# Performance work log

Hardware: AMD Instinct MI355X
Metric: run time of the kernel (lower is better)

The kernel has to match this reference:

```python
import jax, jax.numpy as jnp
import numpy as np

# --- module constants (from init_kwargs) ---
CIN, COUT = 16, 8
HIN = WIN = 8
K, S, P, OP = 3, 2, 1, 1
GRID_SIZE, SPLINE_ORDER = 5, 3
HOUT = (HIN - 1) * S - 2 * P + K + OP  # 16
WOUT = HOUT
OH_IN = (HIN + 2 * P - K) // S + 1   # 4
OW_IN = OH_IN
OH_OUT = (HOUT + 2 * P - K) // S + 1  # 8
OW_OUT = OH_OUT
IN_F = CIN * K * K * OH_IN * OW_IN    # 2304
OUT_F = COUT * K * K * OH_OUT * OW_OUT  # 4608
B = 64


def make_grid():
    h = (1.0 - (-1.0)) / GRID_SIZE
    g = jnp.arange(-SPLINE_ORDER, GRID_SIZE + SPLINE_ORDER + 1, dtype=jnp.float32) * h - 1.0
    return jnp.broadcast_to(g, (IN_F, g.shape[0]))  # [in_features, G+2k+1]


def unfold(x):
    # x: [B, C, H, W] -> [B, C*K*K, OH*OW], torch F.unfold ordering (C, kh, kw) x (oh, ow)
    b, c, h, w = x.shape
    xp = jnp.pad(x, ((0, 0), (0, 0), (P, P), (P, P)))
    oh = (h + 2 * P - K) // S + 1
    ow = (w + 2 * P - K) // S + 1
    patches = jnp.stack(
        [xp[:, :, i:i + (oh - 1) * S + 1:S, j:j + (ow - 1) * S + 1:S]
         for i in range(K) for j in range(K)], axis=2)  # [B, C, K*K, oh, ow]
    return patches.reshape(b, c * K * K, oh * ow)


def fold(u, out_h, out_w):
    # u: [B, C*K*K, oh*ow] -> scatter-add -> [B, C, out_h, out_w] (torch F.fold)
    b = u.shape[0]
    c = u.shape[1] // (K * K)
    oh = (out_h + 2 * P - K) // S + 1
    ow = (out_w + 2 * P - K) // S + 1
    u = u.reshape(b, c, K, K, oh, ow)
    out = jnp.zeros((b, c, out_h + 2 * P, out_w + 2 * P), dtype=u.dtype)
    for i in range(K):
        for j in range(K):
            out = out.at[:, :, i:i + (oh - 1) * S + 1:S, j:j + (ow - 1) * S + 1:S].add(u[:, :, i, j])
    return out[:, :, P:out_h + P, P:out_w + P]


def b_splines(x2, grid):
    # x2: [N, in_f], grid: [in_f, G+2k+1] -> [N, in_f, G+k]
    xg = x2[:, :, None]
    bases = ((xg >= grid[:, :-1]) & (xg < grid[:, 1:])).astype(x2.dtype)
    for k in range(1, SPLINE_ORDER + 1):
        bases = ((xg - grid[:, :-(k + 1)]) / (grid[:, k:-1] - grid[:, :-(k + 1)]) * bases[:, :, :-1]
                 + (grid[:, k + 1:] - xg) / (grid[:, k + 1:] - grid[:, 1:-k]) * bases[:, :, 1:])
    return bases


def setup_inputs() -> dict:
    key = jax.random.key(0)
    k1, k2, k3, k4 = jax.random.split(key, 4)
    return {
        "x": jax.random.normal(k1, (B, CIN, HIN, WIN), dtype=jnp.float32),
        "base_weight": jax.random.normal(k2, (OUT_F, IN_F), dtype=jnp.float32) * 0.02,
        "spline_weight": jax.random.normal(k3, (OUT_F, IN_F, GRID_SIZE + SPLINE_ORDER), dtype=jnp.float32) * 0.02,
        "spline_scaler": jax.random.normal(k4, (OUT_F, IN_F), dtype=jnp.float32) * 0.02,
        "grid": make_grid(),
    }


def reference(x, base_weight, spline_weight, spline_scaler, grid):
    u = unfold(x).reshape(-1, IN_F)  # [B, in_features]
    # KANLinear: base path (SiLU + linear) + spline path
    base_out = jax.nn.silu(u) @ base_weight.T  # [B, out_f]
    scaled_w = (spline_weight * spline_scaler[:, :, None]).reshape(OUT_F, -1)
    spline_out = b_splines(u, grid).reshape(u.shape[0], -1) @ scaled_w.T
    y = (base_out + spline_out).reshape(-1, COUT * K * K, OH_OUT * OW_OUT)
    return fold(y, HOUT, WOUT)  # [B, COUT, HOUT, WOUT]
```

## Files before the change

### kernel.cpp

```cpp
#include <hip/hip_runtime.h>

#define CIN   16
#define COUTC 8
#define HIN   8
#define WINW  8
#define SST   2
#define PPD   1
#define HOUTC 16
#define WOUTC 16
#define IN_F  2304
#define OUT_F 4608
#define BATCH 64

#define OS    8
#define FC    (IN_F / OS)
#define SF    16
#define NSUB  (FC / SF)
#define NWAVE 3

typedef __bf16 bf16x8 __attribute__((ext_vector_type(8)));
typedef float  f32x4  __attribute__((ext_vector_type(4)));

__device__ __forceinline__ float gridv(int t) {
    return (float)(t - 3) * 0.4f - 1.0f;
}

__device__ __forceinline__ void gload_lds16(const float* g, float* l) {
    __builtin_amdgcn_global_load_lds(
        (const __attribute__((address_space(1))) unsigned int*)g,
        (__attribute__((address_space(3))) unsigned int*)l, 16, 0, 0);
}

__global__ __launch_bounds__(256) void prep_kernel(const float* __restrict__ x,
                                                   __bf16* __restrict__ Abb,
                                                   __bf16* __restrict__ Bsb) {
    int tid = blockIdx.x * 256 + threadIdx.x;
    if (tid >= IN_F * BATCH) return;
    int f = tid >> 6, b = tid & 63;
    int ckk = f >> 4, s = f & 15;
    int c = ckk / 9, r = ckk % 9;
    int ki = r / 3, kj = r % 3;
    int oh = s >> 2, ow = s & 3;
    int h = ki + oh * SST - PPD;
    int w = kj + ow * SST - PPD;
    float u = 0.0f;
    if (h >= 0 && h < HIN && w >= 0 && w < WINW)
        u = x[((b * CIN + c) * HIN + h) * WINW + w];

    {
        size_t idx = ((size_t)((f >> 5) * 4 + (b >> 4))) * 512
                   + (((f >> 3) & 3) * 16 + (b & 15)) * 8 + (f & 7);
        Abb[idx] = (__bf16)(u / (1.0f + __expf(-u)));
    }

    float bs[11];
#pragma unroll
    for (int t = 0; t < 11; ++t)
        bs[t] = (u >= gridv(t) && u < gridv(t + 1)) ? 1.0f : 0.0f;
#pragma unroll
    for (int k = 1; k <= 3; ++k) {
#pragma unroll
        for (int i = 0; i < 11; ++i) {
            if (i < 11 - k) {
                float g_i  = gridv(i);
                float g_ik = gridv(i + k);
                float g_i1 = gridv(i + 1);
                float g_k1 = gridv(i + k + 1);
                bs[i] = (u - g_i) / (g_ik - g_i) * bs[i]
                      + (g_k1 - u) / (g_k1 - g_i1) * bs[i + 1];
            }
        }
    }
    bf16x8 v;
#pragma unroll
    for (int t = 0; t < 8; ++t) v[t] = (__bf16)bs[t];
    size_t frag = ((size_t)((f >> 2) * 4 + (b >> 4))) * 64
                + (f & 3) * 16 + (b & 15);
    ((bf16x8*)Bsb)[frag] = v;
}

__global__ __launch_bounds__(192, 2) void gemm_kernel(
    const float* __restrict__ Wb,
    const float* __restrict__ Ws,
    const float* __restrict__ Sc,
    const __bf16* __restrict__ Abb,
    const __bf16* __restrict__ Bsb,
    float* __restrict__ partial)
{
    __shared__ __align__(16) char smem[2 * 16384 + 2 * 4096];
    char* splb = smem;
    char* scb  = smem + 32768;

    const int tid  = threadIdx.x;
    const int lane = tid & 63;
    const int wv   = tid >> 6;
    const int lr   = lane & 15;
    const int lg   = lane >> 4;
    const int ot = blockIdx.x / OS;
    const int os = blockIdx.x % OS;
    const int o0 = ot * 48;
    const int f0 = os * FC;
    const int o  = o0 + wv * 16 + lr;

    f32x4 acc0 = {0.f,0.f,0.f,0.f}, acc1 = {0.f,0.f,0.f,0.f};
    f32x4 acc2 = {0.f,0.f,0.f,0.f}, acc3 = {0.f,0.f,0.f,0.f};

    auto stage = [&](int t, int pb) {
        const char* src = (const char*)Bsb + ((size_t)(f0 + t * SF) >> 2) * 4096;
        char* dst = splb + pb * 16384;
        for (int i = wv; i < 16; i += NWAVE)
            gload_lds16((const float*)(src + i * 1024) + lane * 4,
                        (float*)(dst + i * 1024));
        const int r = wv * 16 + (lane >> 2);
        gload_lds16(Sc + (size_t)(o0 + r) * IN_F + f0 + t * SF + (lane & 3) * 4,
                    (float*)(scb + pb * 4096 + wv * 1024));
    };

    const float* wp = Ws + ((size_t)o * IN_F + f0 + lg) * 8;

    stage(0, 0);
    __syncthreads();

    for (int t = 0; t < NSUB; ++t) {
        const int pb = t & 1;
        if (t + 1 < NSUB) stage(t + 1, pb ^ 1);

        const char*  ab  = splb + pb * 16384;
        const float* scl = (const float*)(scb + pb * 4096);
#pragma unroll
        for (int s = 0; s < SF / 4; ++s) {
            const int fs = t * SF + s * 4;
            float4 w0 = *(const float4*)(wp + (size_t)fs * 8);
            float4 w1 = *(const float4*)(wp + (size_t)fs * 8 + 4);
            float  sc = scl[(wv * 16 + lr) * 16 + s * 4 + lg];
            bf16x8 b0 = *(const bf16x8*)(ab + s * 4096 +    0 + lane * 16);
            bf16x8 b1 = *(const bf16x8*)(ab + s * 4096 + 1024 + lane * 16);
            bf16x8 b2 = *(const bf16x8*)(ab + s * 4096 + 2048 + lane * 16);
            bf16x8 b3 = *(const bf16x8*)(ab + s * 4096 + 3072 + lane * 16);
            bf16x8 af;
            af[0] = (__bf16)(w0.x * sc); af[1] = (__bf16)(w0.y * sc);
            af[2] = (__bf16)(w0.z * sc); af[3] = (__bf16)(w0.w * sc);
            af[4] = (__bf16)(w1.x * sc); af[5] = (__bf16)(w1.y * sc);
            af[6] = (__bf16)(w1.z * sc); af[7] = (__bf16)(w1.w * sc);
            acc0 = __builtin_amdgcn_mfma_f32_16x16x32_bf16(af, b0, acc0, 0, 0, 0);
            acc1 = __builtin_amdgcn_mfma_f32_16x16x32_bf16(af, b1, acc1, 0, 0, 0);
            acc2 = __builtin_amdgcn_mfma_f32_16x16x32_bf16(af, b2, acc2, 0, 0, 0);
            acc3 = __builtin_amdgcn_mfma_f32_16x16x32_bf16(af, b3, acc3, 0, 0, 0);
        }
        __syncthreads();
    }

    const float*  wbp = Wb + (size_t)o * IN_F + f0 + lg * 8;
    const bf16x8* ap  = (const bf16x8*)Abb + ((size_t)f0 >> 5) * 256 + lane;
#pragma unroll
    for (int s = 0; s < FC / 32; ++s) {
        float4 w0 = *(const float4*)(wbp + s * 32);
        float4 w1 = *(const float4*)(wbp + s * 32 + 4);
        bf16x8 b0 = ap[s * 256 +   0];
        bf16x8 b1 = ap[s * 256 +  64];
        bf16x8 b2 = ap[s * 256 + 128];
        bf16x8 b3 = ap[s * 256 + 192];
        bf16x8 af;
        af[0] = (__bf16)w0.x; af[1] = (__bf16)w0.y;
        af[2] = (__bf16)w0.z; af[3] = (__bf16)w0.w;
        af[4] = (__bf16)w1.x; af[5] = (__bf16)w1.y;
        af[6] = (__bf16)w1.z; af[7] = (__bf16)w1.w;
        acc0 = __builtin_amdgcn_mfma_f32_16x16x32_bf16(af, b0, acc0, 0, 0, 0);
        acc1 = __builtin_amdgcn_mfma_f32_16x16x32_bf16(af, b1, acc1, 0, 0, 0);
        acc2 = __builtin_amdgcn_mfma_f32_16x16x32_bf16(af, b2, acc2, 0, 0, 0);
        acc3 = __builtin_amdgcn_mfma_f32_16x16x32_bf16(af, b3, acc3, 0, 0, 0);
    }

#pragma unroll
    for (int r = 0; r < 4; ++r) {
        const size_t row = (size_t)os * OUT_F + o0 + wv * 16 + lg * 4 + r;
        partial[row * 64 +  0 + lr] = acc0[r];
        partial[row * 64 + 16 + lr] = acc1[r];
        partial[row * 64 + 32 + lr] = acc2[r];
        partial[row * 64 + 48 + lr] = acc3[r];
    }
}

__global__ __launch_bounds__(256) void fold_kernel(const float* __restrict__ partial,
                                                   float* __restrict__ out) {
    int gid = blockIdx.x * 256 + threadIdx.x;
    int b = gid & 63, p = gid >> 6;
    int w = p & 15, h = (p >> 4) & 15, c = p >> 8;
    float sum = 0.0f;
#pragma unroll
    for (int ki = 0; ki < 3; ++ki) {
        int th = h + 1 - ki;
        if (th < 0 || (th & 1) || (th >> 1) >= 8) continue;
        int oh = th >> 1;
#pragma unroll
        for (int kj = 0; kj < 3; ++kj) {
            int tw = w + 1 - kj;
            if (tw < 0 || (tw & 1) || (tw >> 1) >= 8) continue;
            int ow = tw >> 1;
            int o = ((c * 3 + ki) * 3 + kj) * 64 + oh * 8 + ow;
            const float* pp = partial + (size_t)o * 64 + b;
#pragma unroll
            for (int os = 0; os < OS; ++os)
                sum += pp[(size_t)os * (OUT_F * 64)];
        }
    }
    out[((b * COUTC + c) * HOUTC + h) * WOUTC + w] = sum;
}

extern "C" void kernel_launch(void* const* d_in, const int* in_sizes, int n_in,
                              void* d_out, int out_size, void* d_ws, size_t ws_size,
                              hipStream_t stream) {
    const float* x  = (const float*)d_in[0];
    const float* Wb = (const float*)d_in[1];
    const float* Ws = (const float*)d_in[2];
    const float* Sc = (const float*)d_in[3];

    float* out = (float*)d_out;

    __bf16* Abb     = (__bf16*)d_ws;
    __bf16* Bsb     = Abb + (size_t)IN_F * BATCH;
    float*  partial = (float*)(Bsb + (size_t)IN_F * BATCH * 8);

    prep_kernel<<<(IN_F * BATCH + 255) / 256, 256, 0, stream>>>(x, Abb, Bsb);

    gemm_kernel<<<(OUT_F / 48) * OS, 192, 0, stream>>>(Wb, Ws, Sc, Abb, Bsb, partial);

    fold_kernel<<<(BATCH * COUTC * HOUTC * WOUTC) / 256, 256, 0, stream>>>(partial, out);
}
```

Measured before the change: 104.2 us.

## Double split-K factor, halve sub-tile, and raise GEMM occupancy

Doubles the K-split from 8 to 16 slices and halves the per-step feature chunk, so the grid has twice as many GEMM blocks and each block uses less LDS. Launch bounds now allow 5 blocks per SIMD instead of 2. The scaler tile is loaded once every two sub-steps and double-buffered separately, and the base-path 32-feature blocks are spread unevenly (5 or 4 per slice) because 72 blocks do not divide by 16. The aim is more memory parallelism on the bandwidth-bound weight stream. The cost is twice the partial-sum traffic written by the GEMM and read back by the fold kernel.

```diff
diff --git a/kernel.cpp b/kernel.cpp
--- a/kernel.cpp
+++ b/kernel.cpp
@@ -12,9 +12,9 @@
 #define OUT_F 4608
 #define BATCH 64
 
-#define OS    8
+#define OS    16
 #define FC    (IN_F / OS)
-#define SF    16
+#define SF    8
 #define NSUB  (FC / SF)
 #define NWAVE 3
 
@@ -79,7 +79,7 @@
     ((bf16x8*)Bsb)[frag] = v;
 }
 
-__global__ __launch_bounds__(192, 2) void gemm_kernel(
+__global__ __launch_bounds__(192, 5) void gemm_kernel(
     const float* __restrict__ Wb,
     const float* __restrict__ Ws,
     const float* __restrict__ Sc,
@@ -87,9 +87,9 @@
     const __bf16* __restrict__ Bsb,
     float* __restrict__ partial)
 {
-    __shared__ __align__(16) char smem[2 * 16384 + 2 * 4096];
-    char* splb = smem;
-    char* scb  = smem + 32768;
+    __shared__ __align__(16) char smem[2 * 8192 + 2 * 3072];
+    char*  splb = smem;
+    float* scb  = (float*)(smem + 16384);
 
     const int tid  = threadIdx.x;
     const int lane = tid & 63;
@@ -105,34 +105,39 @@
     f32x4 acc0 = {0.f,0.f,0.f,0.f}, acc1 = {0.f,0.f,0.f,0.f};
     f32x4 acc2 = {0.f,0.f,0.f,0.f}, acc3 = {0.f,0.f,0.f,0.f};
 
-    auto stage = [&](int t, int pb) {
-        const char* src = (const char*)Bsb + ((size_t)(f0 + t * SF) >> 2) * 4096;
-        char* dst = splb + pb * 16384;
-        for (int i = wv; i < 16; i += NWAVE)
+    auto stage_act = [&](int t, int pb) {
+        const char* src = (const char*)Bsb + (size_t)(f0 + t * SF) * 1024;
+        char* dst = splb + pb * 8192;
+        for (int i = wv; i < 8; i += NWAVE)
             gload_lds16((const float*)(src + i * 1024) + lane * 4,
                         (float*)(dst + i * 1024));
+    };
+    auto stage_sc = [&](int t) {
         const int r = wv * 16 + (lane >> 2);
         gload_lds16(Sc + (size_t)(o0 + r) * IN_F + f0 + t * SF + (lane & 3) * 4,
-                    (float*)(scb + pb * 4096 + wv * 1024));
+                    scb + ((t >> 1) & 1) * 768 + wv * 256);
     };
 
     const float* wp = Ws + ((size_t)o * IN_F + f0 + lg) * 8;
 
-    stage(0, 0);
+    stage_act(0, 0);
+    stage_sc(0);
     __syncthreads();
 
     for (int t = 0; t < NSUB; ++t) {
         const int pb = t & 1;
-        if (t + 1 < NSUB) stage(t + 1, pb ^ 1);
-
-        const char*  ab  = splb + pb * 16384;
-        const float* scl = (const float*)(scb + pb * 4096);
+        if (t + 1 < NSUB) {
+            stage_act(t + 1, pb ^ 1);
+            if (((t + 1) & 1) == 0) stage_sc(t + 1);
+        }
+
+        const char*  ab  = splb + pb * 8192;
+        const float* scl = scb + ((t >> 1) & 1) * 768;
 #pragma unroll
         for (int s = 0; s < SF / 4; ++s) {
-            const int fs = t * SF + s * 4;
-            float4 w0 = *(const float4*)(wp + (size_t)fs * 8);
-            float4 w1 = *(const float4*)(wp + (size_t)fs * 8 + 4);
-            float  sc = scl[(wv * 16 + lr) * 16 + s * 4 + lg];
+            float4 w0 = *(const float4*)(wp + (size_t)(t * SF + s * 4) * 8);
+            float4 w1 = *(const float4*)(wp + (size_t)(t * SF + s * 4) * 8 + 4);
+            float  sc = scl[(wv * 16 + lr) * 16 + (t & 1) * 8 + s * 4 + lg];
             bf16x8 b0 = *(const bf16x8*)(ab + s * 4096 +    0 + lane * 16);
             bf16x8 b1 = *(const bf16x8*)(ab + s * 4096 + 1024 + lane * 16);
             bf16x8 b2 = *(const bf16x8*)(ab + s * 4096 + 2048 + lane * 16);
@@ -150,16 +155,18 @@
         __syncthreads();
     }
 
-    const float*  wbp = Wb + (size_t)o * IN_F + f0 + lg * 8;
-    const bf16x8* ap  = (const bf16x8*)Abb + ((size_t)f0 >> 5) * 256 + lane;
-#pragma unroll
-    for (int s = 0; s < FC / 32; ++s) {
-        float4 w0 = *(const float4*)(wbp + s * 32);
-        float4 w1 = *(const float4*)(wbp + s * 32 + 4);
-        bf16x8 b0 = ap[s * 256 +   0];
-        bf16x8 b1 = ap[s * 256 +  64];
-        bf16x8 b2 = ap[s * 256 + 128];
-        bf16x8 b3 = ap[s * 256 + 192];
+    const int nbs = (os < 8) ? 5 : 4;
+    const int sb0 = (os < 8) ? os * 5 : 40 + (os - 8) * 4;
+    for (int s = 0; s < nbs; ++s) {
+        const int fb = (sb0 + s) * 32;
+        const float* wbp = Wb + (size_t)o * IN_F + fb + lg * 8;
+        const bf16x8* ap = (const bf16x8*)Abb + ((size_t)fb >> 5) * 256 + lane;
+        float4 w0 = *(const float4*)wbp;
+        float4 w1 = *(const float4*)(wbp + 4);
+        bf16x8 b0 = ap[0];
+        bf16x8 b1 = ap[64];
+        bf16x8 b2 = ap[128];
+        bf16x8 b3 = ap[192];
         bf16x8 af;
         af[0] = (__bf16)w0.x; af[1] = (__bf16)w0.y;
         af[2] = (__bf16)w0.z; af[3] = (__bf16)w0.w;
@@ -200,8 +207,8 @@
             int o = ((c * 3 + ki) * 3 + kj) * 64 + oh * 8 + ow;
             const float* pp = partial + (size_t)o * 64 + b;
 #pragma unroll
-            for (int os = 0; os < OS; ++os)
-                sum += pp[(size_t)os * (OUT_F * 64)];
+            for (int osl = 0; osl < OS; ++osl)
+                sum += pp[(size_t)osl * (OUT_F * 64)];
         }
     }
     out[((b * COUTC + c) * HOUTC + h) * WOUTC + w] = sum;
```

Result: slower. 112.5 us (+8.0%).

## Stage spline weights through swizzled LDS with async loads, halve sub-tile size

Applied to the files above, without the earlier changes.

The spline-weight tile is now staged into LDS through async global-to-LDS loads with an XOR swizzle, double-buffered alongside the activation and scaler tiles. Before, each lane read it directly from global memory with float4 loads. The sub-tile shrinks from 16 to 8 features so the three buffers fit in LDS, and the scaler staging moves to two waves. The aim is to overlap the dominant weight stream with MFMA work and get coalesced fetches, at the cost of more loop iterations and barriers.

```diff
diff --git a/kernel.cpp b/kernel.cpp
--- a/kernel.cpp
+++ b/kernel.cpp
@@ -14,7 +14,7 @@
 
 #define OS    8
 #define FC    (IN_F / OS)
-#define SF    16
+#define SF    8
 #define NSUB  (FC / SF)
 #define NWAVE 3
 
@@ -87,9 +87,10 @@
     const __bf16* __restrict__ Bsb,
     float* __restrict__ partial)
 {
-    __shared__ __align__(16) char smem[2 * 16384 + 2 * 4096];
-    char* splb = smem;
-    char* scb  = smem + 32768;
+    __shared__ __align__(16) char smem[2 * 12288 + 2 * 8192 + 2 * 1536];
+    char*  wlds = smem;
+    char*  alds = smem + 24576;
+    float* scb  = (float*)(smem + 40960);
 
     const int tid  = threadIdx.x;
     const int lane = tid & 63;
@@ -101,38 +102,71 @@
     const int o0 = ot * 48;
     const int f0 = os * FC;
     const int o  = o0 + wv * 16 + lr;
+    const int R  = wv * 16 + lr;
 
     f32x4 acc0 = {0.f,0.f,0.f,0.f}, acc1 = {0.f,0.f,0.f,0.f};
     f32x4 acc2 = {0.f,0.f,0.f,0.f}, acc3 = {0.f,0.f,0.f,0.f};
 
-    auto stage = [&](int t, int pb) {
-        const char* src = (const char*)Bsb + ((size_t)(f0 + t * SF) >> 2) * 4096;
-        char* dst = splb + pb * 16384;
-        for (int i = wv; i < 16; i += NWAVE)
+    auto stage_w = [&](int t, int pb) {
+        const int fs = f0 + t * SF;
+        char* dst = wlds + pb * 12288;
+#pragma unroll
+        for (int k = 0; k < 4; ++k) {
+            const int q  = wv + k * NWAVE;
+            const int rq = q * 4 + (lane >> 4);
+            const float* row = Ws + ((size_t)(o0 + rq) * IN_F + fs) * 8;
+            const int su = (lane & 15) ^ (rq & 7);
+            gload_lds16(row + su * 4, (float*)(dst + q * 1024));
+        }
+    };
+    auto stage_act = [&](int t, int pb) {
+        const char* src = (const char*)Bsb + (size_t)(f0 + t * SF) * 1024;
+        char* dst = alds + pb * 8192;
+        for (int i = wv; i < 8; i += NWAVE)
             gload_lds16((const float*)(src + i * 1024) + lane * 4,
                         (float*)(dst + i * 1024));
-        const int r = wv * 16 + (lane >> 2);
-        gload_lds16(Sc + (size_t)(o0 + r) * IN_F + f0 + t * SF + (lane & 3) * 4,
-                    (float*)(scb + pb * 4096 + wv * 1024));
-    };
-
-    const float* wp = Ws + ((size_t)o * IN_F + f0 + lg) * 8;
-
-    stage(0, 0);
+    };
+    auto stage_sc = [&](int t, int pb) {
+        const int r  = wv * 16 + ((lane & 31) >> 1);
+        const int fq = (lane & 1) * 4;
+        gload_lds16(Sc + (size_t)(o0 + r) * IN_F + f0 + t * SF + fq,
+                    (float*)(scb + ((pb) ? 384 : 0)) + wv * 128
+                    );
+    };
+    (void)stage_sc;
+
+    auto stage_sc2 = [&](int t, int pb) {
+        if (wv < 2) {
+            const int r  = wv * 32 + (lane >> 1);
+            const int fq = (lane & 1) * 4;
+            gload_lds16(Sc + (size_t)(o0 + r) * IN_F + f0 + t * SF + fq,
+                        (float*)(scb) + pb * 384 + wv * 256);
+        }
+    };
+
+    stage_w(0, 0);
+    stage_act(0, 0);
+    stage_sc2(0, 0);
     __syncthreads();
 
     for (int t = 0; t < NSUB; ++t) {
         const int pb = t & 1;
-        if (t + 1 < NSUB) stage(t + 1, pb ^ 1);
-
-        const char*  ab  = splb + pb * 16384;
-        const float* scl = (const float*)(scb + pb * 4096);
+        if (t + 1 < NSUB) {
+            stage_w(t + 1, pb ^ 1);
+            stage_act(t + 1, pb ^ 1);
+            stage_sc2(t + 1, pb ^ 1);
+        }
+
+        const char*  wb_  = wlds + pb * 12288;
+        const char*  ab   = alds + pb * 8192;
+        const float* scl  = scb + pb * 384;
 #pragma unroll
         for (int s = 0; s < SF / 4; ++s) {
-            const int fs = t * SF + s * 4;
-            float4 w0 = *(const float4*)(wp + (size_t)fs * 8);
-            float4 w1 = *(const float4*)(wp + (size_t)fs * 8 + 4);
-            float  sc = scl[(wv * 16 + lr) * 16 + s * 4 + lg];
+            const int j0 = (8 * s + 2 * lg)     ^ (R & 7);
+            const int j1 = (8 * s + 2 * lg + 1) ^ (R & 7);
+            float4 w0 = *(const float4*)(wb_ + R * 256 + j0 * 16);
+            float4 w1 = *(const float4*)(wb_ + R * 256 + j1 * 16);
+            float  sc = scl[R * 8 + s * 4 + lg];
             bf16x8 b0 = *(const bf16x8*)(ab + s * 4096 +    0 + lane * 16);
             bf16x8 b1 = *(const bf16x8*)(ab + s * 4096 + 1024 + lane * 16);
             bf16x8 b2 = *(const bf16x8*)(ab + s * 4096 + 2048 + lane * 16);
@@ -200,8 +234,8 @@
             int o = ((c * 3 + ki) * 3 + kj) * 64 + oh * 8 + ow;
             const float* pp = partial + (size_t)o * 64 + b;
 #pragma unroll
-            for (int os = 0; os < OS; ++os)
-                sum += pp[(size_t)os * (OUT_F * 64)];
+            for (int osl = 0; osl < OS; ++osl)
+                sum += pp[(size_t)osl * (OUT_F * 64)];
         }
     }
     out[((b * COUTC + c) * HOUTC + h) * WOUTC + w] = sum;
```

Result: no change. 105.4 us (+1.2%).
